# Performance work log

Hardware: AMD Instinct MI355X
Metric: run time of the kernel (lower is better)

Reference implementation:

```python
import jax, jax.numpy as jnp
import numpy as np

B, T, D_MODEL, HEAD_SIZE = 8, 1024, 1024, 64
BLOCK_SIZE = 1024  # == max_relative_pos


def setup_inputs() -> dict:
    key = jax.random.key(0)
    ks = jax.random.split(key, 7)
    s = 1.0 / np.sqrt(D_MODEL)
    return {
        "x": jax.random.normal(ks[0], (B, T, D_MODEL), dtype=jnp.float32),
        "Wk": jax.random.normal(ks[1], (D_MODEL, HEAD_SIZE), dtype=jnp.float32) * s,
        "bk": jax.random.normal(ks[2], (HEAD_SIZE,), dtype=jnp.float32) * 0.02,
        "Wq": jax.random.normal(ks[3], (D_MODEL, HEAD_SIZE), dtype=jnp.float32) * s,
        "bq": jax.random.normal(ks[4], (HEAD_SIZE,), dtype=jnp.float32) * 0.02,
        "Wv": jax.random.normal(ks[5], (D_MODEL, HEAD_SIZE), dtype=jnp.float32) * s,
        "rel_emb": jax.random.normal(ks[6], (2 * BLOCK_SIZE + 1, HEAD_SIZE), dtype=jnp.float32) * 0.02,
        "mask": 1,
    }


def reference(x, Wk, bk, Wq, bq, Wv, rel_emb, mask):
    Bb, Tt, _ = x.shape
    hs = Wk.shape[1]
    max_rel = (rel_emb.shape[0] - 1) // 2

    k = x @ Wk + bk          # [B,T,hs]
    q = x @ Wq + bq          # [B,T,hs]
    v = x @ Wv               # [B,T,hs]

    pos = jnp.arange(Tt)
    idx = jnp.clip(pos[:, None] - pos[None, :], -max_rel, max_rel) + max_rel
    r = rel_emb[idx]         # [T,T,hs], r[i,j] = emb(clip(i-j))

    # scores[b,i,j] = (q[b,i] + r[i,j]) . (k[b,j] + r[j,i]) / sqrt(hs)
    scale = 1.0 / np.sqrt(hs).astype(np.float32)
    scores = (
        jnp.einsum("bid,bjd->bij", q, k)
        + jnp.einsum("bid,jid->bij", q, r)   # q_i . r[j,i]
        + jnp.einsum("ijd,bjd->bij", r, k)   # r[i,j] . k_j
        + jnp.einsum("ijd,jid->ij", r, r)[None]  # r[i,j] . r[j,i]
    ) * scale

    if mask:  # static Python int -> causal mask, matches tril masked_fill
        causal = jnp.tril(jnp.ones((Tt, Tt), dtype=bool))
        scores = jnp.where(causal, scores, jnp.float32(-jnp.inf))

    w = jax.nn.softmax(scores, axis=-1)  # dropout is identity in eval mode
    return w @ v  # [B,T,hs]
```

## Files before the change

### kernel.cpp

```cpp
#include <hip/hip_runtime.h>
#include <hip/hip_bf16.h>
#include <math.h>


typedef __hip_bfloat16 bf16;
typedef __attribute__((ext_vector_type(8))) short short8;
typedef __attribute__((ext_vector_type(4))) float f32x4;

#define NTRI 136
#define MFMA16(a, b, c) __builtin_amdgcn_mfma_f32_16x16x32_bf16(a, b, c, 0, 0, 0)

__device__ __forceinline__ float bf2f(bf16 h) { return __bfloat162float(h); }
__device__ __forceinline__ bf16 f2bf(float f) { return __float2bfloat16(f); }
__device__ __forceinline__ short bfs(float f) {
  bf16 h = __float2bfloat16(f);
  return *(short*)&h;
}

union U16 {
  uint4 u;
  short8 s;
};
__device__ __forceinline__ short8 ldfrag(const bf16* p) {
  U16 x;
  x.u = *(const uint4*)p;
  return x.s;
}

__global__ __launch_bounds__(256) void prep_kernel(
    const float* __restrict__ Wk, const float* __restrict__ Wq, const float* __restrict__ Wv,
    const float* __restrict__ E, bf16* __restrict__ WT, bf16* __restrict__ Ep,
    bf16* __restrict__ Erev, float* __restrict__ rrG, float* __restrict__ zeroBase) {
  const int bid = blockIdx.x, t = threadIdx.x;
  if (bid < 768) {
    int idx = bid * 256 + t;
    int sel = idx >> 16, r = idx & 65535;
    int n = r >> 10, kk = r & 1023;
    const float* W = (sel == 0) ? Wk : (sel == 1) ? Wq : Wv;
    WT[idx] = f2bf(W[kk * 64 + n]);
  } else if (bid < 1281) {
    int idx = (bid - 768) * 256 + t;
    if (idx < 2049 * 64) {
      int tt = idx >> 6, d = idx & 63;
      Ep[idx] = f2bf(E[idx]);
      Erev[idx] = f2bf(E[(size_t)(2048 - tt) * 64 + d]);
    }
  } else if (bid < 1537) {
    int dlt = ((bid - 1281) << 2) + (t >> 6);
    int d = t & 63;
    float p = E[(size_t)(1024 + dlt) * 64 + d] * E[(size_t)(1024 - dlt) * 64 + d];
#pragma unroll
    for (int off = 32; off > 0; off >>= 1) p += __shfl_down(p, off);
    if (d == 0) rrG[64 + dlt] = p;
  } else {
    int idx4 = (bid - 1537) * 256 + t;
    if (idx4 * 4 < 532480)
      *(float4*)(zeroBase + idx4 * 4) = make_float4(0.f, 0.f, 0.f, 0.f);
  }
}

__global__ __launch_bounds__(256, 2) void qkv_mfma(
    const float* __restrict__ x, const bf16* __restrict__ WT,
    const float* __restrict__ bk, const float* __restrict__ bq,
    bf16* __restrict__ qB, bf16* __restrict__ kB, bf16* __restrict__ vT) {
  const int R0 = blockIdx.x << 4;
  const int t = threadIdx.x;
  const int lane = t & 63, wave = t >> 6;
  const int m = lane & 15, quad = lane >> 4;

  __shared__ float RED[4][16][196];
  __shared__ bf16 VTS[64][24];

  const float* xrow = x + (size_t)(R0 + m) * 1024 + (wave << 8);
  f32x4 acc[3][4];
#pragma unroll
  for (int s = 0; s < 3; ++s)
#pragma unroll
    for (int c = 0; c < 4; ++c) acc[s][c] = (f32x4){0.f, 0.f, 0.f, 0.f};

#pragma unroll
  for (int ks = 0; ks < 8; ++ks) {
    const int k0 = ks * 32 + quad * 8;
    float4 xa = *(const float4*)(xrow + k0);
    float4 xb = *(const float4*)(xrow + k0 + 4);
    short8 a;
    a[0] = bfs(xa.x); a[1] = bfs(xa.y); a[2] = bfs(xa.z); a[3] = bfs(xa.w);
    a[4] = bfs(xb.x); a[5] = bfs(xb.y); a[6] = bfs(xb.z); a[7] = bfs(xb.w);
    const int kg = (wave << 8) + k0;
#pragma unroll
    for (int sel = 0; sel < 3; ++sel)
#pragma unroll
      for (int ct = 0; ct < 4; ++ct) {
        const bf16* bb = WT + ((size_t)(sel * 64 + ct * 16 + m) << 10) + kg;
        acc[sel][ct] = MFMA16(a, ldfrag(bb), acc[sel][ct]);
      }
  }

#pragma unroll
  for (int sel = 0; sel < 3; ++sel)
#pragma unroll
    for (int ct = 0; ct < 4; ++ct)
#pragma unroll
      for (int r = 0; r < 4; ++r)
        RED[wave][quad * 4 + r][sel * 64 + ct * 16 + m] = acc[sel][ct][r];
  __syncthreads();

#pragma unroll
  for (int e = 0; e < 12; ++e) {
    int idx = e * 256 + t;
    int row = idx / 192, c = idx - row * 192;
    float s = RED[0][row][c] + RED[1][row][c] + RED[2][row][c] + RED[3][row][c];
    int sel = c >> 6, col = c & 63;
    size_t grow = (size_t)(R0 + row);
    if (sel == 0) kB[grow * 64 + col] = f2bf(s + bk[col]);
    else if (sel == 1) qB[grow * 64 + col] = f2bf(s + bq[col]);
    else VTS[col][row] = f2bf(s);
  }
  __syncthreads();
  {
    int dd = t >> 2, h = (t & 3) << 2;
    int b = R0 >> 10, tloc = R0 & 1023;
    *(uint2*)(vT + ((size_t)((b << 6) + dd) << 10) + tloc + h) = *(const uint2*)&VTS[dd][h];
  }
}

__global__ __launch_bounds__(256, 2) void flash_mfma(
    const bf16* __restrict__ qB, const bf16* __restrict__ kB, const bf16* __restrict__ vT,
    const bf16* __restrict__ Ep, const bf16* __restrict__ Erev, const float* __restrict__ rrG,
    float* __restrict__ Oacc, float* __restrict__ Lacc) {
  const int bx = blockIdx.x;
  const int b = bx / NTRI;
  const int rr_ = bx - b * NTRI;
  int it = (int)((sqrtf(8.f * rr_ + 1.f) - 1.f) * 0.5f);
  while ((it + 1) * (it + 2) / 2 <= rr_) ++it;
  while (it * (it + 1) / 2 > rr_) --it;
  const int jt = rr_ - it * (it + 1) / 2;
  const int I0 = it << 6, J0 = jt << 6;
  const int D = I0 - J0, w0 = D - 64;

  const int t = threadIdx.x;
  const int lane = t & 63, wave = t >> 6;
  const int m = lane & 15, quad = lane >> 4;
  const int strip = wave << 4;

  __shared__ __align__(16) bf16 M2S[64][136];
  __shared__ bf16 M3S[64][136];
  bf16 (*PS)[80] = (bf16(*)[80])M2S;

  const bf16* qbase = qB + ((size_t)((b << 10) + I0 + strip + m) << 6);
  const short8 aq0 = ldfrag(qbase + quad * 8);
  const short8 aq1 = ldfrag(qbase + 32 + quad * 8);
  const bf16* kbase = kB + ((size_t)((b << 10) + J0 + strip + m) << 6);
  const short8 ak0 = ldfrag(kbase + quad * 8);
  const short8 ak1 = ldfrag(kbase + 32 + quad * 8);

  const bf16* erb = Erev + ((size_t)(1024 + w0) << 6);
  const bf16* epb = Ep + ((size_t)(1024 + w0) << 6);
#pragma unroll
  for (int ct = 0; ct < 8; ++ct) {
    const bf16* bb2 = erb + ((size_t)(ct * 16 + m) << 6) + quad * 8;
    const bf16* bb3 = epb + ((size_t)(ct * 16 + m) << 6) + quad * 8;
    const short8 b20 = ldfrag(bb2);
    const short8 b21 = ldfrag(bb2 + 32);
    const short8 b30 = ldfrag(bb3);
    const short8 b31 = ldfrag(bb3 + 32);
    const float rv = rrG[64 + w0 + ct * 16 + m];
    f32x4 c2 = (f32x4){0.f, 0.f, 0.f, 0.f};
    c2 = MFMA16(aq0, b20, c2);
    c2 = MFMA16(aq1, b21, c2);
    f32x4 c3 = (f32x4){0.f, 0.f, 0.f, 0.f};
    c3 = MFMA16(ak0, b30, c3);
    c3 = MFMA16(ak1, b31, c3);
#pragma unroll
    for (int r = 0; r < 4; ++r) {
      M2S[strip + quad * 4 + r][ct * 16 + m] = f2bf(c2[r] + rv);
      M3S[strip + quad * 4 + r][ct * 16 + m] = f2bf(c3[r]);
    }
  }
  f32x4 acc[4];
#pragma unroll
  for (int ct = 0; ct < 4; ++ct) {
    const bf16* bb = kB + ((size_t)((b << 10) + J0 + ct * 16 + m) << 6) + quad * 8;
    f32x4 c = (f32x4){0.f, 0.f, 0.f, 0.f};
    c = MFMA16(aq0, ldfrag(bb), c);
    c = MFMA16(aq1, ldfrag(bb + 32), c);
    acc[ct] = c;
  }
  __syncthreads();

  float sc[4][4], lrow[4] = {0.f, 0.f, 0.f, 0.f};
#pragma unroll
  for (int ct = 0; ct < 4; ++ct) {
    const int uj = ct * 16 + m;
#pragma unroll
    for (int r = 0; r < 4; ++r) {
      const int ui = strip + quad * 4 + r;
      float s;
      if (ui - uj + D >= 0) {
        const int wi = ui - uj + 64;
        s = (acc[ct][r] + bf2f(M2S[ui][wi]) + bf2f(M3S[uj][wi])) * 0.125f;
      } else {
        s = -INFINITY;
      }
      float p = __expf(s - 8.0f);
      sc[ct][r] = p;
      lrow[r] += p;
    }
  }
#pragma unroll
  for (int r = 0; r < 4; ++r) {
#pragma unroll
    for (int off = 1; off < 16; off <<= 1) lrow[r] += __shfl_xor(lrow[r], off);
  }
  if (m == 0) {
#pragma unroll
    for (int r = 0; r < 4; ++r)
      atomicAdd(&Lacc[(b << 10) + I0 + strip + quad * 4 + r], lrow[r]);
  }
  __syncthreads();
#pragma unroll
  for (int ct = 0; ct < 4; ++ct)
#pragma unroll
    for (int r = 0; r < 4; ++r) PS[strip + quad * 4 + r][ct * 16 + m] = f2bf(sc[ct][r]);
  __syncthreads();

  const short8 ap0 = ldfrag(&PS[strip + m][quad * 8]);
  const short8 ap1 = ldfrag(&PS[strip + m][32 + quad * 8]);
  float* ob = Oacc + ((size_t)((b << 10) + I0) << 6);
#pragma unroll
  for (int ct = 0; ct < 4; ++ct) {
    const bf16* bb = vT + ((size_t)(b * 64 + ct * 16 + m) << 10) + J0 + quad * 8;
    f32x4 o = (f32x4){0.f, 0.f, 0.f, 0.f};
    o = MFMA16(ap0, ldfrag(bb), o);
    o = MFMA16(ap1, ldfrag(bb + 32), o);
#pragma unroll
    for (int r = 0; r < 4; ++r)
      atomicAdd(&ob[(size_t)(strip + quad * 4 + r) * 64 + ct * 16 + m], o[r]);
  }
}

__global__ __launch_bounds__(256) void normalize_kernel(
    const float* __restrict__ Oacc, const float* __restrict__ Lacc, float* __restrict__ out) {
  int idx = blockIdx.x * 256 + threadIdx.x;
  out[idx] = Oacc[idx] / Lacc[idx >> 6];
}

extern "C" void kernel_launch(void* const* d_in, const int* in_sizes, int n_in,
                              void* d_out, int out_size, void* d_ws, size_t ws_size,
                              hipStream_t stream) {
  const float* x = (const float*)d_in[0];
  const float* Wk = (const float*)d_in[1];
  const float* bk = (const float*)d_in[2];
  const float* Wq = (const float*)d_in[3];
  const float* bq = (const float*)d_in[4];
  const float* Wv = (const float*)d_in[5];
  const float* E = (const float*)d_in[6];
  float* out = (float*)d_out;

  float* wsf = (float*)d_ws;
  float* Oacc = wsf;
  float* Lacc = wsf + 524288;
  float* rrG = wsf + 532480;
  bf16* qB = (bf16*)(rrG + 1152);
  bf16* kB = qB + 524288;
  bf16* vT = kB + 524288;
  bf16* Ep = vT + 524288;
  bf16* Erev = Ep + 131200;
  bf16* WT = Erev + 131200;

  prep_kernel<<<2058, 256, 0, stream>>>(Wk, Wq, Wv, E, WT, Ep, Erev, rrG, Oacc);
  qkv_mfma<<<512, 256, 0, stream>>>(x, WT, bk, bq, qB, kB, vT);
  flash_mfma<<<8 * NTRI, 256, 0, stream>>>(qB, kB, vT, Ep, Erev, rrG, Oacc, Lacc);
  normalize_kernel<<<2048, 256, 0, stream>>>(Oacc, Lacc, out);
}
```

Measured before the change: 148.6 us.

## Precompute relative-position score terms once into global tables, drop per-tile recomputation

Adds a relgemm kernel that computes q·Erev and k·Ep (plus the rr bias) for every row and every relative distance in 0..1023, once, into two bf16 global tables of size B*T*1024. The flash kernel then gathers these per-element values from global memory instead of recomputing 128-wide relative GEMMs per tile into shared memory. It also makes the P staging per-wave so the block-wide barriers can go. The cost is about 32 MB of extra global writes and scattered reads, which may be limited by memory bandwidth.

```diff
diff --git a/kernel.cpp b/kernel.cpp
--- a/kernel.cpp
+++ b/kernel.cpp
@@ -124,9 +124,47 @@
   }
 }
 
+__global__ __launch_bounds__(256, 2) void relgemm_kernel(
+    const bf16* __restrict__ qB, const bf16* __restrict__ kB,
+    const bf16* __restrict__ Ep, const bf16* __restrict__ Erev,
+    const float* __restrict__ rrG, bf16* __restrict__ M2G, bf16* __restrict__ M3G) {
+  const int R0 = blockIdx.x << 4;
+  const int t = threadIdx.x;
+  const int lane = t & 63, wave = t >> 6;
+  const int m = lane & 15, quad = lane >> 4;
+  const int d0 = wave << 8;
+
+  const bf16* qrow = qB + ((size_t)(R0 + m) << 6);
+  const bf16* krow = kB + ((size_t)(R0 + m) << 6);
+  const short8 aq0 = ldfrag(qrow + quad * 8);
+  const short8 aq1 = ldfrag(qrow + 32 + quad * 8);
+  const short8 ak0 = ldfrag(krow + quad * 8);
+  const short8 ak1 = ldfrag(krow + 32 + quad * 8);
+
+#pragma unroll
+  for (int ct = 0; ct < 16; ++ct) {
+    const int dlt = d0 + ct * 16 + m;
+    const bf16* b2 = Erev + ((size_t)(1024 + dlt) << 6) + quad * 8;
+    const bf16* b3 = Ep + ((size_t)(1024 + dlt) << 6) + quad * 8;
+    f32x4 c2 = (f32x4){0.f, 0.f, 0.f, 0.f};
+    c2 = MFMA16(aq0, ldfrag(b2), c2);
+    c2 = MFMA16(aq1, ldfrag(b2 + 32), c2);
+    f32x4 c3 = (f32x4){0.f, 0.f, 0.f, 0.f};
+    c3 = MFMA16(ak0, ldfrag(b3), c3);
+    c3 = MFMA16(ak1, ldfrag(b3 + 32), c3);
+    const float rv = rrG[64 + dlt];
+#pragma unroll
+    for (int r = 0; r < 4; ++r) {
+      const size_t o = ((size_t)(R0 + quad * 4 + r) << 10) + dlt;
+      M2G[o] = f2bf(c2[r] + rv);
+      M3G[o] = f2bf(c3[r]);
+    }
+  }
+}
+
 __global__ __launch_bounds__(256, 2) void flash_mfma(
     const bf16* __restrict__ qB, const bf16* __restrict__ kB, const bf16* __restrict__ vT,
-    const bf16* __restrict__ Ep, const bf16* __restrict__ Erev, const float* __restrict__ rrG,
+    const bf16* __restrict__ M2G, const bf16* __restrict__ M3G,
     float* __restrict__ Oacc, float* __restrict__ Lacc) {
   const int bx = blockIdx.x;
   const int b = bx / NTRI;
@@ -136,47 +174,19 @@
   while (it * (it + 1) / 2 > rr_) --it;
   const int jt = rr_ - it * (it + 1) / 2;
   const int I0 = it << 6, J0 = jt << 6;
-  const int D = I0 - J0, w0 = D - 64;
+  const int D = I0 - J0;
 
   const int t = threadIdx.x;
   const int lane = t & 63, wave = t >> 6;
   const int m = lane & 15, quad = lane >> 4;
   const int strip = wave << 4;
 
-  __shared__ __align__(16) bf16 M2S[64][136];
-  __shared__ bf16 M3S[64][136];
-  bf16 (*PS)[80] = (bf16(*)[80])M2S;
+  __shared__ __align__(16) bf16 PS[4][16][80];
 
   const bf16* qbase = qB + ((size_t)((b << 10) + I0 + strip + m) << 6);
   const short8 aq0 = ldfrag(qbase + quad * 8);
   const short8 aq1 = ldfrag(qbase + 32 + quad * 8);
-  const bf16* kbase = kB + ((size_t)((b << 10) + J0 + strip + m) << 6);
-  const short8 ak0 = ldfrag(kbase + quad * 8);
-  const short8 ak1 = ldfrag(kbase + 32 + quad * 8);
-
-  const bf16* erb = Erev + ((size_t)(1024 + w0) << 6);
-  const bf16* epb = Ep + ((size_t)(1024 + w0) << 6);
-#pragma unroll
-  for (int ct = 0; ct < 8; ++ct) {
-    const bf16* bb2 = erb + ((size_t)(ct * 16 + m) << 6) + quad * 8;
-    const bf16* bb3 = epb + ((size_t)(ct * 16 + m) << 6) + quad * 8;
-    const short8 b20 = ldfrag(bb2);
-    const short8 b21 = ldfrag(bb2 + 32);
-    const short8 b30 = ldfrag(bb3);
-    const short8 b31 = ldfrag(bb3 + 32);
-    const float rv = rrG[64 + w0 + ct * 16 + m];
-    f32x4 c2 = (f32x4){0.f, 0.f, 0.f, 0.f};
-    c2 = MFMA16(aq0, b20, c2);
-    c2 = MFMA16(aq1, b21, c2);
-    f32x4 c3 = (f32x4){0.f, 0.f, 0.f, 0.f};
-    c3 = MFMA16(ak0, b30, c3);
-    c3 = MFMA16(ak1, b31, c3);
-#pragma unroll
-    for (int r = 0; r < 4; ++r) {
-      M2S[strip + quad * 4 + r][ct * 16 + m] = f2bf(c2[r] + rv);
-      M3S[strip + quad * 4 + r][ct * 16 + m] = f2bf(c3[r]);
-    }
-  }
+
   f32x4 acc[4];
 #pragma unroll
   for (int ct = 0; ct < 4; ++ct) {
@@ -186,7 +196,6 @@
     c = MFMA16(aq1, ldfrag(bb + 32), c);
     acc[ct] = c;
   }
-  __syncthreads();
 
   float sc[4][4], lrow[4] = {0.f, 0.f, 0.f, 0.f};
 #pragma unroll
@@ -195,14 +204,16 @@
 #pragma unroll
     for (int r = 0; r < 4; ++r) {
       const int ui = strip + quad * 4 + r;
-      float s;
-      if (ui - uj + D >= 0) {
-        const int wi = ui - uj + 64;
-        s = (acc[ct][r] + bf2f(M2S[ui][wi]) + bf2f(M3S[uj][wi])) * 0.125f;
+      const int dl = ui - uj + D;
+      float p;
+      if (dl >= 0) {
+        const float m2 = bf2f(M2G[((size_t)((b << 10) + I0 + ui) << 10) + dl]);
+        const float m3 = bf2f(M3G[((size_t)((b << 10) + J0 + uj) << 10) + dl]);
+        const float s = (acc[ct][r] + m2 + m3) * 0.125f;
+        p = __expf(s - 8.0f);
       } else {
-        s = -INFINITY;
+        p = 0.0f;
       }
-      float p = __expf(s - 8.0f);
       sc[ct][r] = p;
       lrow[r] += p;
     }
@@ -217,15 +228,14 @@
     for (int r = 0; r < 4; ++r)
       atomicAdd(&Lacc[(b << 10) + I0 + strip + quad * 4 + r], lrow[r]);
   }
-  __syncthreads();
+
 #pragma unroll
   for (int ct = 0; ct < 4; ++ct)
 #pragma unroll
-    for (int r = 0; r < 4; ++r) PS[strip + quad * 4 + r][ct * 16 + m] = f2bf(sc[ct][r]);
-  __syncthreads();
-
-  const short8 ap0 = ldfrag(&PS[strip + m][quad * 8]);
-  const short8 ap1 = ldfrag(&PS[strip + m][32 + quad * 8]);
+    for (int r = 0; r < 4; ++r) PS[wave][quad * 4 + r][ct * 16 + m] = f2bf(sc[ct][r]);
+
+  const short8 ap0 = ldfrag(&PS[wave][m][quad * 8]);
+  const short8 ap1 = ldfrag(&PS[wave][m][32 + quad * 8]);
   float* ob = Oacc + ((size_t)((b << 10) + I0) << 6);
 #pragma unroll
   for (int ct = 0; ct < 4; ++ct) {
@@ -267,9 +277,12 @@
   bf16* Ep = vT + 524288;
   bf16* Erev = Ep + 131200;
   bf16* WT = Erev + 131200;
+  bf16* M2G = WT + 196608;
+  bf16* M3G = M2G + 8388608;
 
   prep_kernel<<<2058, 256, 0, stream>>>(Wk, Wq, Wv, E, WT, Ep, Erev, rrG, Oacc);
   qkv_mfma<<<512, 256, 0, stream>>>(x, WT, bk, bq, qB, kB, vT);
-  flash_mfma<<<8 * NTRI, 256, 0, stream>>>(qB, kB, vT, Ep, Erev, rrG, Oacc, Lacc);
+  relgemm_kernel<<<512, 256, 0, stream>>>(qB, kB, Ep, Erev, rrG, M2G, M3G);
+  flash_mfma<<<8 * NTRI, 256, 0, stream>>>(qB, kB, vT, M2G, M3G, Oacc, Lacc);
   normalize_kernel<<<2048, 256, 0, stream>>>(Oacc, Lacc, out);
 }
```

After: 163.0 us. 1.1x slower.

## Group up to four key tiles per block and accumulate output in registers

Applied to the files above, without the earlier changes.

Each flash block now handles one query tile against a chunk of up to four key tiles, looping over them instead of getting a single (i,j) tile pair. The P@V result is accumulated in registers across the chunk, so global float atomics to Oacc and Lacc are issued once per chunk rather than once per tile pair. P is staged in a per-wave shared buffer, which drops one barrier per tile. This cuts atomic traffic and repeated Q loads, but the grid shrinks from 1088 to 320 blocks, work per block becomes uneven (1 to 4 tiles), and each block runs its tiles serially.

```diff
diff --git a/kernel.cpp b/kernel.cpp
--- a/kernel.cpp
+++ b/kernel.cpp
@@ -7,7 +7,7 @@
 typedef __attribute__((ext_vector_type(8))) short short8;
 typedef __attribute__((ext_vector_type(4))) float f32x4;
 
-#define NTRI 136
+#define NCHUNK 40
 #define MFMA16(a, b, c) __builtin_amdgcn_mfma_f32_16x16x32_bf16(a, b, c, 0, 0, 0)
 
 __device__ __forceinline__ float bf2f(bf16 h) { return __bfloat162float(h); }
@@ -129,14 +129,19 @@
     const bf16* __restrict__ Ep, const bf16* __restrict__ Erev, const float* __restrict__ rrG,
     float* __restrict__ Oacc, float* __restrict__ Lacc) {
   const int bx = blockIdx.x;
-  const int b = bx / NTRI;
-  const int rr_ = bx - b * NTRI;
-  int it = (int)((sqrtf(8.f * rr_ + 1.f) - 1.f) * 0.5f);
-  while ((it + 1) * (it + 2) / 2 <= rr_) ++it;
-  while (it * (it + 1) / 2 > rr_) --it;
-  const int jt = rr_ - it * (it + 1) / 2;
-  const int I0 = it << 6, J0 = jt << 6;
-  const int D = I0 - J0, w0 = D - 64;
+  const int b = bx / NCHUNK;
+  const int rr2 = bx - b * NCHUNK;
+  int it = 15, chunk = 0;
+  {
+    int acc0 = 0;
+    for (int k = 15; k >= 0; --k) {
+      int c = (k >> 2) + 1;
+      if (rr2 < acc0 + c) { it = k; chunk = rr2 - acc0; break; }
+      acc0 += c;
+    }
+  }
+  const int ntiles = min(4, it + 1 - (chunk << 2));
+  const int I0 = it << 6;
 
   const int t = threadIdx.x;
   const int lane = t & 63, wave = t >> 6;
@@ -145,68 +150,96 @@
 
   __shared__ __align__(16) bf16 M2S[64][136];
   __shared__ bf16 M3S[64][136];
-  bf16 (*PS)[80] = (bf16(*)[80])M2S;
+  __shared__ __align__(16) bf16 PS[4][16][80];
 
   const bf16* qbase = qB + ((size_t)((b << 10) + I0 + strip + m) << 6);
   const short8 aq0 = ldfrag(qbase + quad * 8);
   const short8 aq1 = ldfrag(qbase + 32 + quad * 8);
-  const bf16* kbase = kB + ((size_t)((b << 10) + J0 + strip + m) << 6);
-  const short8 ak0 = ldfrag(kbase + quad * 8);
-  const short8 ak1 = ldfrag(kbase + 32 + quad * 8);
-
-  const bf16* erb = Erev + ((size_t)(1024 + w0) << 6);
-  const bf16* epb = Ep + ((size_t)(1024 + w0) << 6);
-#pragma unroll
-  for (int ct = 0; ct < 8; ++ct) {
-    const bf16* bb2 = erb + ((size_t)(ct * 16 + m) << 6) + quad * 8;
-    const bf16* bb3 = epb + ((size_t)(ct * 16 + m) << 6) + quad * 8;
-    const short8 b20 = ldfrag(bb2);
-    const short8 b21 = ldfrag(bb2 + 32);
-    const short8 b30 = ldfrag(bb3);
-    const short8 b31 = ldfrag(bb3 + 32);
-    const float rv = rrG[64 + w0 + ct * 16 + m];
-    f32x4 c2 = (f32x4){0.f, 0.f, 0.f, 0.f};
-    c2 = MFMA16(aq0, b20, c2);
-    c2 = MFMA16(aq1, b21, c2);
-    f32x4 c3 = (f32x4){0.f, 0.f, 0.f, 0.f};
-    c3 = MFMA16(ak0, b30, c3);
-    c3 = MFMA16(ak1, b31, c3);
-#pragma unroll
-    for (int r = 0; r < 4; ++r) {
-      M2S[strip + quad * 4 + r][ct * 16 + m] = f2bf(c2[r] + rv);
-      M3S[strip + quad * 4 + r][ct * 16 + m] = f2bf(c3[r]);
-    }
-  }
-  f32x4 acc[4];
-#pragma unroll
-  for (int ct = 0; ct < 4; ++ct) {
-    const bf16* bb = kB + ((size_t)((b << 10) + J0 + ct * 16 + m) << 6) + quad * 8;
-    f32x4 c = (f32x4){0.f, 0.f, 0.f, 0.f};
-    c = MFMA16(aq0, ldfrag(bb), c);
-    c = MFMA16(aq1, ldfrag(bb + 32), c);
-    acc[ct] = c;
-  }
-  __syncthreads();
-
-  float sc[4][4], lrow[4] = {0.f, 0.f, 0.f, 0.f};
-#pragma unroll
-  for (int ct = 0; ct < 4; ++ct) {
-    const int uj = ct * 16 + m;
-#pragma unroll
-    for (int r = 0; r < 4; ++r) {
-      const int ui = strip + quad * 4 + r;
-      float s;
-      if (ui - uj + D >= 0) {
-        const int wi = ui - uj + 64;
-        s = (acc[ct][r] + bf2f(M2S[ui][wi]) + bf2f(M3S[uj][wi])) * 0.125f;
-      } else {
-        s = -INFINITY;
+
+  f32x4 osum[4];
+#pragma unroll
+  for (int ct = 0; ct < 4; ++ct) osum[ct] = (f32x4){0.f, 0.f, 0.f, 0.f};
+  float lrow[4] = {0.f, 0.f, 0.f, 0.f};
+
+  for (int s = 0; s < ntiles; ++s) {
+    const int jt = (chunk << 2) + s;
+    const int J0 = jt << 6;
+    const int D = I0 - J0, w0 = D - 64;
+
+    const bf16* kbase = kB + ((size_t)((b << 10) + J0 + strip + m) << 6);
+    const short8 ak0 = ldfrag(kbase + quad * 8);
+    const short8 ak1 = ldfrag(kbase + 32 + quad * 8);
+
+    const bf16* erb = Erev + ((size_t)(1024 + w0) << 6);
+    const bf16* epb = Ep + ((size_t)(1024 + w0) << 6);
+#pragma unroll
+    for (int ct = 0; ct < 8; ++ct) {
+      const bf16* bb2 = erb + ((size_t)(ct * 16 + m) << 6) + quad * 8;
+      const bf16* bb3 = epb + ((size_t)(ct * 16 + m) << 6) + quad * 8;
+      const short8 b20 = ldfrag(bb2);
+      const short8 b21 = ldfrag(bb2 + 32);
+      const short8 b30 = ldfrag(bb3);
+      const short8 b31 = ldfrag(bb3 + 32);
+      const float rv = rrG[64 + w0 + ct * 16 + m];
+      f32x4 c2 = (f32x4){0.f, 0.f, 0.f, 0.f};
+      c2 = MFMA16(aq0, b20, c2);
+      c2 = MFMA16(aq1, b21, c2);
+      f32x4 c3 = (f32x4){0.f, 0.f, 0.f, 0.f};
+      c3 = MFMA16(ak0, b30, c3);
+      c3 = MFMA16(ak1, b31, c3);
+#pragma unroll
+      for (int r = 0; r < 4; ++r) {
+        M2S[strip + quad * 4 + r][ct * 16 + m] = f2bf(c2[r] + rv);
+        M3S[strip + quad * 4 + r][ct * 16 + m] = f2bf(c3[r]);
       }
-      float p = __expf(s - 8.0f);
-      sc[ct][r] = p;
-      lrow[r] += p;
-    }
-  }
+    }
+    f32x4 acc[4];
+#pragma unroll
+    for (int ct = 0; ct < 4; ++ct) {
+      const bf16* bb = kB + ((size_t)((b << 10) + J0 + ct * 16 + m) << 6) + quad * 8;
+      f32x4 c = (f32x4){0.f, 0.f, 0.f, 0.f};
+      c = MFMA16(aq0, ldfrag(bb), c);
+      c = MFMA16(aq1, ldfrag(bb + 32), c);
+      acc[ct] = c;
+    }
+    __syncthreads();
+
+    float sc[4][4];
+#pragma unroll
+    for (int ct = 0; ct < 4; ++ct) {
+      const int uj = ct * 16 + m;
+#pragma unroll
+      for (int r = 0; r < 4; ++r) {
+        const int ui = strip + quad * 4 + r;
+        float p;
+        if (ui - uj + D >= 0) {
+          const int wi = ui - uj + 64;
+          const float sv = (acc[ct][r] + bf2f(M2S[ui][wi]) + bf2f(M3S[uj][wi])) * 0.125f;
+          p = __expf(sv - 8.0f);
+        } else {
+          p = 0.0f;
+        }
+        sc[ct][r] = p;
+        lrow[r] += p;
+      }
+    }
+    __syncthreads();
+
+#pragma unroll
+    for (int ct = 0; ct < 4; ++ct)
+#pragma unroll
+      for (int r = 0; r < 4; ++r) PS[wave][quad * 4 + r][ct * 16 + m] = f2bf(sc[ct][r]);
+
+    const short8 ap0 = ldfrag(&PS[wave][m][quad * 8]);
+    const short8 ap1 = ldfrag(&PS[wave][m][32 + quad * 8]);
+#pragma unroll
+    for (int ct = 0; ct < 4; ++ct) {
+      const bf16* bb = vT + ((size_t)(b * 64 + ct * 16 + m) << 10) + J0 + quad * 8;
+      osum[ct] = MFMA16(ap0, ldfrag(bb), osum[ct]);
+      osum[ct] = MFMA16(ap1, ldfrag(bb + 32), osum[ct]);
+    }
+  }
+
 #pragma unroll
   for (int r = 0; r < 4; ++r) {
 #pragma unroll
@@ -217,26 +250,12 @@
     for (int r = 0; r < 4; ++r)
       atomicAdd(&Lacc[(b << 10) + I0 + strip + quad * 4 + r], lrow[r]);
   }
-  __syncthreads();
+  float* ob = Oacc + ((size_t)((b << 10) + I0) << 6);
 #pragma unroll
   for (int ct = 0; ct < 4; ++ct)
 #pragma unroll
-    for (int r = 0; r < 4; ++r) PS[strip + quad * 4 + r][ct * 16 + m] = f2bf(sc[ct][r]);
-  __syncthreads();
-
-  const short8 ap0 = ldfrag(&PS[strip + m][quad * 8]);
-  const short8 ap1 = ldfrag(&PS[strip + m][32 + quad * 8]);
-  float* ob = Oacc + ((size_t)((b << 10) + I0) << 6);
-#pragma unroll
-  for (int ct = 0; ct < 4; ++ct) {
-    const bf16* bb = vT + ((size_t)(b * 64 + ct * 16 + m) << 10) + J0 + quad * 8;
-    f32x4 o = (f32x4){0.f, 0.f, 0.f, 0.f};
-    o = MFMA16(ap0, ldfrag(bb), o);
-    o = MFMA16(ap1, ldfrag(bb + 32), o);
-#pragma unroll
     for (int r = 0; r < 4; ++r)
-      atomicAdd(&ob[(size_t)(strip + quad * 4 + r) * 64 + ct * 16 + m], o[r]);
-  }
+      atomicAdd(&ob[(size_t)(strip + quad * 4 + r) * 64 + ct * 16 + m], osum[ct][r]);
 }
 
 __global__ __launch_bounds__(256) void normalize_kernel(
@@ -270,6 +289,6 @@
 
   prep_kernel<<<2058, 256, 0, stream>>>(Wk, Wq, Wv, E, WT, Ep, Erev, rrG, Oacc);
   qkv_mfma<<<512, 256, 0, stream>>>(x, WT, bk, bq, qB, kB, vT);
-  flash_mfma<<<8 * NTRI, 256, 0, stream>>>(qB, kB, vT, Ep, Erev, rrG, Oacc, Lacc);
+  flash_mfma<<<8 * NCHUNK, 256, 0, stream>>>(qB, kB, vT, Ep, Erev, rrG, Oacc, Lacc);
   normalize_kernel<<<2048, 256, 0, stream>>>(Oacc, Lacc, out);
 }
```

Result: slower. 164.1 us (+10.4%).

## Shrink attention tiles to 32x32 per wave and drop block barriers

Applied to the files above, without the earlier changes.

The flash kernel now assigns one 32x32 causal (i,j) tile to each wave instead of one 64x64 tile per 256-thread block. Each wave gets its own shared-memory scratch, so all __syncthreads are removed, and launch bounds rise to 4 blocks per SM. The aim is less wasted work on the masked diagonal, with barrier stalls and occupancy limits removed. In exchange there are about twice as many atomicAdds to Oacc and Lacc, and more redundant rel-emb fragment loads per unit of output.

```diff
diff --git a/kernel.cpp b/kernel.cpp
--- a/kernel.cpp
+++ b/kernel.cpp
@@ -7,7 +7,7 @@
 typedef __attribute__((ext_vector_type(8))) short short8;
 typedef __attribute__((ext_vector_type(4))) float f32x4;
 
-#define NTRI 136
+#define NTILE32 528
 #define MFMA16(a, b, c) __builtin_amdgcn_mfma_f32_16x16x32_bf16(a, b, c, 0, 0, 0)
 
 __device__ __forceinline__ float bf2f(bf16 h) { return __bfloat162float(h); }
@@ -124,118 +124,140 @@
   }
 }
 
-__global__ __launch_bounds__(256, 2) void flash_mfma(
+__global__ __launch_bounds__(256, 4) void flash_mfma(
     const bf16* __restrict__ qB, const bf16* __restrict__ kB, const bf16* __restrict__ vT,
     const bf16* __restrict__ Ep, const bf16* __restrict__ Erev, const float* __restrict__ rrG,
     float* __restrict__ Oacc, float* __restrict__ Lacc) {
-  const int bx = blockIdx.x;
-  const int b = bx / NTRI;
-  const int rr_ = bx - b * NTRI;
-  int it = (int)((sqrtf(8.f * rr_ + 1.f) - 1.f) * 0.5f);
-  while ((it + 1) * (it + 2) / 2 <= rr_) ++it;
-  while (it * (it + 1) / 2 > rr_) --it;
-  const int jt = rr_ - it * (it + 1) / 2;
-  const int I0 = it << 6, J0 = jt << 6;
-  const int D = I0 - J0, w0 = D - 64;
-
   const int t = threadIdx.x;
   const int lane = t & 63, wave = t >> 6;
   const int m = lane & 15, quad = lane >> 4;
-  const int strip = wave << 4;
-
-  __shared__ __align__(16) bf16 M2S[64][136];
-  __shared__ bf16 M3S[64][136];
-  bf16 (*PS)[80] = (bf16(*)[80])M2S;
-
-  const bf16* qbase = qB + ((size_t)((b << 10) + I0 + strip + m) << 6);
-  const short8 aq0 = ldfrag(qbase + quad * 8);
-  const short8 aq1 = ldfrag(qbase + 32 + quad * 8);
-  const bf16* kbase = kB + ((size_t)((b << 10) + J0 + strip + m) << 6);
-  const short8 ak0 = ldfrag(kbase + quad * 8);
-  const short8 ak1 = ldfrag(kbase + 32 + quad * 8);
+
+  const int g = (blockIdx.x << 2) + wave;
+  const int b = g / NTILE32;
+  const int r0 = g - b * NTILE32;
+  int it = (int)((sqrtf(8.f * r0 + 1.f) - 1.f) * 0.5f);
+  while ((it + 1) * (it + 2) / 2 <= r0) ++it;
+  while (it * (it + 1) / 2 > r0) --it;
+  const int jt = r0 - it * (it + 1) / 2;
+  const int I0 = it << 5, J0 = jt << 5;
+  const int D = I0 - J0, w0 = D - 32;
+
+  __shared__ __align__(16) bf16 M2S[4][32][68];
+  __shared__ __align__(16) bf16 M3S[4][32][68];
+  bf16 (*M2)[68] = M2S[wave];
+  bf16 (*M3)[68] = M3S[wave];
+  bf16 (*PS)[40] = (bf16(*)[40]) & M3S[wave][0][0];
+
+  const bf16* qb = qB + ((size_t)((b << 10) + I0) << 6);
+  const bf16* kb = kB + ((size_t)((b << 10) + J0) << 6);
+  short8 aq[2][2], kf[2][2];
+#pragma unroll
+  for (int rt = 0; rt < 2; ++rt)
+#pragma unroll
+    for (int ks = 0; ks < 2; ++ks) {
+      aq[rt][ks] = ldfrag(qb + ((rt * 16 + m) << 6) + ks * 32 + quad * 8);
+      kf[rt][ks] = ldfrag(kb + ((rt * 16 + m) << 6) + ks * 32 + quad * 8);
+    }
 
   const bf16* erb = Erev + ((size_t)(1024 + w0) << 6);
   const bf16* epb = Ep + ((size_t)(1024 + w0) << 6);
 #pragma unroll
-  for (int ct = 0; ct < 8; ++ct) {
-    const bf16* bb2 = erb + ((size_t)(ct * 16 + m) << 6) + quad * 8;
-    const bf16* bb3 = epb + ((size_t)(ct * 16 + m) << 6) + quad * 8;
-    const short8 b20 = ldfrag(bb2);
-    const short8 b21 = ldfrag(bb2 + 32);
-    const short8 b30 = ldfrag(bb3);
-    const short8 b31 = ldfrag(bb3 + 32);
+  for (int ct = 0; ct < 4; ++ct) {
+    const bf16* b2p = erb + ((size_t)(ct * 16 + m) << 6) + quad * 8;
+    const bf16* b3p = epb + ((size_t)(ct * 16 + m) << 6) + quad * 8;
+    const short8 b20 = ldfrag(b2p);
+    const short8 b21 = ldfrag(b2p + 32);
+    const short8 b30 = ldfrag(b3p);
+    const short8 b31 = ldfrag(b3p + 32);
     const float rv = rrG[64 + w0 + ct * 16 + m];
-    f32x4 c2 = (f32x4){0.f, 0.f, 0.f, 0.f};
-    c2 = MFMA16(aq0, b20, c2);
-    c2 = MFMA16(aq1, b21, c2);
-    f32x4 c3 = (f32x4){0.f, 0.f, 0.f, 0.f};
-    c3 = MFMA16(ak0, b30, c3);
-    c3 = MFMA16(ak1, b31, c3);
+#pragma unroll
+    for (int rt = 0; rt < 2; ++rt) {
+      f32x4 c2 = (f32x4){0.f, 0.f, 0.f, 0.f};
+      c2 = MFMA16(aq[rt][0], b20, c2);
+      c2 = MFMA16(aq[rt][1], b21, c2);
+      f32x4 c3 = (f32x4){0.f, 0.f, 0.f, 0.f};
+      c3 = MFMA16(kf[rt][0], b30, c3);
+      c3 = MFMA16(kf[rt][1], b31, c3);
+#pragma unroll
+      for (int r = 0; r < 4; ++r) {
+        M2[rt * 16 + quad * 4 + r][ct * 16 + m] = f2bf(c2[r] + rv);
+        M3[rt * 16 + quad * 4 + r][ct * 16 + m] = f2bf(c3[r]);
+      }
+    }
+  }
+
+  f32x4 acc[2][2];
+#pragma unroll
+  for (int rt = 0; rt < 2; ++rt)
+#pragma unroll
+    for (int ct = 0; ct < 2; ++ct) {
+      f32x4 c = (f32x4){0.f, 0.f, 0.f, 0.f};
+      c = MFMA16(aq[rt][0], kf[ct][0], c);
+      c = MFMA16(aq[rt][1], kf[ct][1], c);
+      acc[rt][ct] = c;
+    }
+
+  float sc[2][2][4], lr[2][4];
+#pragma unroll
+  for (int rt = 0; rt < 2; ++rt)
+#pragma unroll
+    for (int r = 0; r < 4; ++r) lr[rt][r] = 0.f;
+#pragma unroll
+  for (int ct = 0; ct < 2; ++ct) {
+    const int uj = ct * 16 + m;
+#pragma unroll
+    for (int rt = 0; rt < 2; ++rt)
+#pragma unroll
+      for (int r = 0; r < 4; ++r) {
+        const int ui = rt * 16 + quad * 4 + r;
+        float p = 0.f;
+        if (ui - uj + D >= 0) {
+          const int wi = ui - uj + 32;
+          const float sv = (acc[rt][ct][r] + bf2f(M2[ui][wi]) + bf2f(M3[uj][wi])) * 0.125f;
+          p = __expf(sv - 8.0f);
+        }
+        sc[ct][rt][r] = p;
+        lr[rt][r] += p;
+      }
+  }
+#pragma unroll
+  for (int rt = 0; rt < 2; ++rt)
 #pragma unroll
     for (int r = 0; r < 4; ++r) {
-      M2S[strip + quad * 4 + r][ct * 16 + m] = f2bf(c2[r] + rv);
-      M3S[strip + quad * 4 + r][ct * 16 + m] = f2bf(c3[r]);
-    }
-  }
-  f32x4 acc[4];
+#pragma unroll
+      for (int off = 1; off < 16; off <<= 1) lr[rt][r] += __shfl_xor(lr[rt][r], off);
+    }
+  if (m == 0) {
+#pragma unroll
+    for (int rt = 0; rt < 2; ++rt)
+#pragma unroll
+      for (int r = 0; r < 4; ++r)
+        atomicAdd(&Lacc[(b << 10) + I0 + rt * 16 + quad * 4 + r], lr[rt][r]);
+  }
+
+#pragma unroll
+  for (int ct = 0; ct < 2; ++ct)
+#pragma unroll
+    for (int rt = 0; rt < 2; ++rt)
+#pragma unroll
+      for (int r = 0; r < 4; ++r)
+        PS[rt * 16 + quad * 4 + r][ct * 16 + m] = f2bf(sc[ct][rt][r]);
+
+  short8 ap[2];
+#pragma unroll
+  for (int rt = 0; rt < 2; ++rt) ap[rt] = ldfrag(&PS[rt * 16 + m][quad * 8]);
+  float* ob = Oacc + ((size_t)((b << 10) + I0) << 6);
 #pragma unroll
   for (int ct = 0; ct < 4; ++ct) {
-    const bf16* bb = kB + ((size_t)((b << 10) + J0 + ct * 16 + m) << 6) + quad * 8;
-    f32x4 c = (f32x4){0.f, 0.f, 0.f, 0.f};
-    c = MFMA16(aq0, ldfrag(bb), c);
-    c = MFMA16(aq1, ldfrag(bb + 32), c);
-    acc[ct] = c;
-  }
-  __syncthreads();
-
-  float sc[4][4], lrow[4] = {0.f, 0.f, 0.f, 0.f};
-#pragma unroll
-  for (int ct = 0; ct < 4; ++ct) {
-    const int uj = ct * 16 + m;
-#pragma unroll
-    for (int r = 0; r < 4; ++r) {
-      const int ui = strip + quad * 4 + r;
-      float s;
-      if (ui - uj + D >= 0) {
-        const int wi = ui - uj + 64;
-        s = (acc[ct][r] + bf2f(M2S[ui][wi]) + bf2f(M3S[uj][wi])) * 0.125f;
-      } else {
-        s = -INFINITY;
-      }
-      float p = __expf(s - 8.0f);
-      sc[ct][r] = p;
-      lrow[r] += p;
-    }
-  }
-#pragma unroll
-  for (int r = 0; r < 4; ++r) {
-#pragma unroll
-    for (int off = 1; off < 16; off <<= 1) lrow[r] += __shfl_xor(lrow[r], off);
-  }
-  if (m == 0) {
-#pragma unroll
-    for (int r = 0; r < 4; ++r)
-      atomicAdd(&Lacc[(b << 10) + I0 + strip + quad * 4 + r], lrow[r]);
-  }
-  __syncthreads();
-#pragma unroll
-  for (int ct = 0; ct < 4; ++ct)
-#pragma unroll
-    for (int r = 0; r < 4; ++r) PS[strip + quad * 4 + r][ct * 16 + m] = f2bf(sc[ct][r]);
-  __syncthreads();
-
-  const short8 ap0 = ldfrag(&PS[strip + m][quad * 8]);
-  const short8 ap1 = ldfrag(&PS[strip + m][32 + quad * 8]);
-  float* ob = Oacc + ((size_t)((b << 10) + I0) << 6);
-#pragma unroll
-  for (int ct = 0; ct < 4; ++ct) {
-    const bf16* bb = vT + ((size_t)(b * 64 + ct * 16 + m) << 10) + J0 + quad * 8;
-    f32x4 o = (f32x4){0.f, 0.f, 0.f, 0.f};
-    o = MFMA16(ap0, ldfrag(bb), o);
-    o = MFMA16(ap1, ldfrag(bb + 32), o);
-#pragma unroll
-    for (int r = 0; r < 4; ++r)
-      atomicAdd(&ob[(size_t)(strip + quad * 4 + r) * 64 + ct * 16 + m], o[r]);
+    const short8 vf = ldfrag(vT + ((size_t)(b * 64 + ct * 16 + m) << 10) + J0 + quad * 8);
+#pragma unroll
+    for (int rt = 0; rt < 2; ++rt) {
+      f32x4 o = (f32x4){0.f, 0.f, 0.f, 0.f};
+      o = MFMA16(ap[rt], vf, o);
+#pragma unroll
+      for (int r = 0; r < 4; ++r)
+        atomicAdd(&ob[(size_t)(rt * 16 + quad * 4 + r) * 64 + ct * 16 + m], o[r]);
+    }
   }
 }
 
@@ -270,6 +292,6 @@
 
   prep_kernel<<<2058, 256, 0, stream>>>(Wk, Wq, Wv, E, WT, Ep, Erev, rrG, Oacc);
   qkv_mfma<<<512, 256, 0, stream>>>(x, WT, bk, bq, qB, kB, vT);
-  flash_mfma<<<8 * NTRI, 256, 0, stream>>>(qB, kB, vT, Ep, Erev, rrG, Oacc, Lacc);
+  flash_mfma<<<1056, 256, 0, stream>>>(qB, kB, vT, Ep, Erev, rrG, Oacc, Lacc);
   normalize_kernel<<<2048, 256, 0, stream>>>(Oacc, Lacc, out);
 }
```

New measurement: 157.7 us. +6.1%, slower.
